# Performance work log

Measured on AMD Instinct MI355X. Metric: run time of the kernel, lower is better.

## Reference

```python
import jax, jax.numpy as jnp
import numpy as np

D_MODEL = 1024
N_HEADS = 16
D_HEAD = D_MODEL // N_HEADS
WIN = 128        # local_window
HALF = WIN // 2  # 64
KW = 2 * WIN     # kv window length per block (half-left + block + half-right)


def setup_inputs() -> dict:
    key = jax.random.key(0)
    ks = jax.random.split(key, 6)
    B, L = 2, 8192
    s = 0.02
    return {
        "x": jax.random.normal(ks[0], (B, L, D_MODEL), dtype=jnp.float32),
        "wq": jax.random.normal(ks[1], (D_MODEL, D_MODEL), dtype=jnp.float32) * s,
        "wk": jax.random.normal(ks[2], (D_MODEL, D_MODEL), dtype=jnp.float32) * s,
        "wv": jax.random.normal(ks[3], (D_MODEL, D_MODEL), dtype=jnp.float32) * s,
        "wo": jax.random.normal(ks[4], (D_MODEL, D_MODEL), dtype=jnp.float32) * s,
        "bo": jax.random.normal(ks[5], (D_MODEL,), dtype=jnp.float32) * s,
    }


def _rotate_half(t):
    t1, t2 = jnp.split(t, 2, axis=-1)
    return jnp.concatenate([-t2, t1], axis=-1)


def _rope(L, dtype):
    inv_freq = 1.0 / (10000.0 ** (jnp.arange(0, D_HEAD, 2, dtype=jnp.float32) / D_HEAD))
    t = jnp.arange(L, dtype=jnp.float32)
    freqs = t[:, None] * inv_freq[None, :]          # [L, D_HEAD/2]
    emb = jnp.concatenate([freqs, freqs], axis=-1)  # [L, D_HEAD]
    return jnp.cos(emb).astype(dtype), jnp.sin(emb).astype(dtype)


def reference(x, wq, wk, wv, wo, bo):
    B, L, D = x.shape
    H, Dh = N_HEADS, D_HEAD
    # projections (torch Linear: x @ W.T)
    q = (x @ wq.T).reshape(B, L, H, Dh).transpose(0, 2, 1, 3)  # [B,H,L,Dh]
    k = (x @ wk.T).reshape(B, L, H, Dh).transpose(0, 2, 1, 3)
    v = (x @ wv.T).reshape(B, L, H, Dh).transpose(0, 2, 1, 3)
    cos, sin = _rope(L, x.dtype)                    # [L, Dh]
    q = q * cos + _rotate_half(q) * sin
    k = k * cos + _rotate_half(k) * sin
    nb = L // WIN
    starts = jnp.arange(nb) * WIN - HALF            # window start per block
    idx = starts[:, None] + jnp.arange(KW)          # [nb, KW] kv indices
    valid = (idx >= 0) & (idx < L)
    idxc = jnp.clip(idx, 0, L - 1)
    kw = k[:, :, idxc]                              # [B,H,nb,KW,Dh]
    vw = v[:, :, idxc]
    qb = q.reshape(B, H, nb, WIN, Dh)
    scores = jnp.einsum('bhnqd,bhnkd->bhnqk', qb, kw) / np.sqrt(Dh).astype(x.dtype)
    scores = jnp.where(valid[None, None, :, None, :], scores, -jnp.inf)
    attn = jax.nn.softmax(scores, axis=-1)
    out = jnp.einsum('bhnqk,bhnkd->bhnqd', attn, vw).reshape(B, H, L, Dh)
    out = out.transpose(0, 2, 1, 3).reshape(B, L, D)
    return out @ wo.T + bo
```

## Files before the change

### kernel.cpp

```cpp
#include <hip/hip_runtime.h>
#include <cstdint>
#include <math.h>

#define L_SEQ 8192
#define DM    1024
#define NQK   2048

typedef unsigned short u16;
typedef __bf16 bf16;
typedef bf16  bf16x8 __attribute__((ext_vector_type(8)));
typedef float f32x4  __attribute__((ext_vector_type(4)));

__device__ __forceinline__ u16 f2bf(float f) {
    unsigned u = __float_as_uint(f);
    u += 0x7fffu + ((u >> 16) & 1u);
    return (u16)(u >> 16);
}

__device__ __forceinline__ f32x4 mfma16(bf16x8 a, bf16x8 b, f32x4 c) {
    return __builtin_amdgcn_mfma_f32_16x16x32_bf16(a, b, c, 0, 0, 0);
}

__device__ __forceinline__ void gld_lds16(const u16* g, u16* l) {
    __builtin_amdgcn_global_load_lds((const __attribute__((address_space(1))) void*)g,
                                     (__attribute__((address_space(3))) void*)l,
                                     16, 0, 0);
}

__global__ void cvt_bf16(const float* __restrict__ src, u16* __restrict__ dst, int n8) {
    int i = blockIdx.x * 256 + threadIdx.x;
    if (i >= n8) return;
    const float4* s4 = (const float4*)src;
    float4 a = s4[2 * i], b = s4[2 * i + 1];
    union { uint4 u; u16 h[8]; } r;
    r.h[0] = f2bf(a.x); r.h[1] = f2bf(a.y); r.h[2] = f2bf(a.z); r.h[3] = f2bf(a.w);
    r.h[4] = f2bf(b.x); r.h[5] = f2bf(b.y); r.h[6] = f2bf(b.z); r.h[7] = f2bf(b.w);
    ((uint4*)dst)[i] = r.u;
}

__global__ void rope_tbl(float2* __restrict__ t) {
    int idx = blockIdx.x * 256 + threadIdx.x;
    int pos = idx >> 5, i = idx & 31;
    float invf = exp2f(-0.4152410118609191f * (float)i);
    float s, c;
    sincosf((float)pos * invf, &s, &c);
    t[idx] = make_float2(c, s);
}


#define QITER(U, WIMM, RD, ST) do {                                            \
    __builtin_amdgcn_s_waitcnt(WIMM);                                          \
    __builtin_amdgcn_sched_barrier(0);                                         \
    __builtin_amdgcn_s_barrier();                                              \
    __builtin_amdgcn_sched_barrier(0);                                         \
    if (RD) {                                                                  \
        _Pragma("unroll")                                                      \
        for (int m = 0; m < 8; m++)                                            \
            fA[(U + 1) & 1][m] = *(const bf16x8*)(SAs + ((U + 1) % 3) * 8192 + aBase + m * 512); \
        _Pragma("unroll")                                                      \
        for (int n = 0; n < 4; n++)                                            \
            fB[(U + 1) & 1][n] = *(const bf16x8*)(SBs + ((U + 1) % 3) * 4096 + bBase + n * 512); \
    }                                                                          \
    if (ST) {                                                                  \
        _Pragma("unroll")                                                      \
        for (int i = 0; i < 4; ++i)                                            \
            gld_lds16(gA[i] + (U + 3) * 32, ldsAt + (U % 3) * 8192 + i * 2048);\
        _Pragma("unroll")                                                      \
        for (int i = 0; i < 2; ++i)                                            \
            gld_lds16(gB[i] + (U + 3) * 32, ldsBt + (U % 3) * 4096 + i * 2048);\
    }                                                                          \
    __builtin_amdgcn_sched_barrier(0);                                         \
    __builtin_amdgcn_s_setprio(1);                                             \
    _Pragma("unroll")                                                          \
    for (int m = 0; m < 8; m++)                                                \
        _Pragma("unroll")                                                      \
        for (int n = 0; n < 4; n++)                                            \
            acc[m][n] = mfma16(fA[(U) & 1][m], fB[(U) & 1][n], acc[m][n]);     \
    __builtin_amdgcn_s_setprio(0);                                             \
    __builtin_amdgcn_sched_barrier(0);                                         \
} while (0)

#define K_LOOP_ALL()                                                           \
    QITER(0,0x0076,1,1);  QITER(1,0x0076,1,1);  QITER(2,0x0076,1,1);           \
    QITER(3,0x0076,1,1);  QITER(4,0x0076,1,1);  QITER(5,0x0076,1,1);           \
    QITER(6,0x0076,1,1);  QITER(7,0x0076,1,1);  QITER(8,0x0076,1,1);           \
    QITER(9,0x0076,1,1);  QITER(10,0x0076,1,1); QITER(11,0x0076,1,1);          \
    QITER(12,0x0076,1,1); QITER(13,0x0076,1,1); QITER(14,0x0076,1,1);          \
    QITER(15,0x0076,1,1); QITER(16,0x0076,1,1); QITER(17,0x0076,1,1);          \
    QITER(18,0x0076,1,1); QITER(19,0x0076,1,1); QITER(20,0x0076,1,1);          \
    QITER(21,0x0076,1,1); QITER(22,0x0076,1,1); QITER(23,0x0076,1,1);          \
    QITER(24,0x0076,1,1); QITER(25,0x0076,1,1); QITER(26,0x0076,1,1);          \
    QITER(27,0x0076,1,1); QITER(28,0x0076,1,1); QITER(29,0x0076,1,0);          \
    QITER(30,0x0070,1,0); QITER(31,0x0070,0,0)

#define GEMM_SETUP()                                                           \
    u16* SAs = smem;                                \
    u16* SBs = smem + 24576;                        \
    const int tid = threadIdx.x;                                               \
    const int lane = tid & 63, w = tid >> 6;                                   \
    const int wm = w >> 1, wn = w & 1;                                         \
    const int quad = lane >> 4, ln = lane & 15;                                \
    const u16* gA[4]; const u16* gB[2];                                        \
    _Pragma("unroll")                                                          \
    for (int i = 0; i < 4; ++i) {                                              \
        int s = i * 256 + tid;                                                 \
        int li = s >> 3, pc = s & 7, lc = pc ^ (li & 7);                       \
        int row = 2 * li + (lc >> 2), kc = lc & 3;                             \
        gA[i] = Ap + (size_t)(m0 + row) * DM + kc * 8;                         \
    }                                                                          \
    _Pragma("unroll")                                                          \
    for (int i = 0; i < 2; ++i) {                                              \
        int s = i * 256 + tid;                                                 \
        int li = s >> 3, pc = s & 7, lc = pc ^ (li & 7);                       \
        int row = 2 * li + (lc >> 2), kc = lc & 3;                             \
        gB[i] = Bp + (size_t)(n0 + row) * DM + kc * 8;                         \
    }                                                                          \
    u16* ldsAt = SAs + tid * 8;                                                \
    u16* ldsBt = SBs + tid * 8;                                                \
    const int l7  = (ln >> 1) & 7;                                             \
    const int pcq = ((ln & 1) * 4 + quad) ^ l7;                                \
    const int aBase = (wm * 64 + (ln >> 1)) * 64 + pcq * 8;                    \
    const int bBase = (wn * 32 + (ln >> 1)) * 64 + pcq * 8;                    \
    const f32x4 fz = {0.f, 0.f, 0.f, 0.f};                                     \
    f32x4 acc[8][4];                                                           \
    _Pragma("unroll")                                                          \
    for (int a = 0; a < 8; a++)                                                \
        _Pragma("unroll")                                                      \
        for (int b = 0; b < 4; b++) acc[a][b] = fz;                            \
    bf16x8 fA[2][8], fB[2][4];                                                 \
                              \
    _Pragma("unroll")                                                          \
    for (int t3 = 0; t3 < 3; ++t3) {                                           \
        _Pragma("unroll")                                                      \
        for (int i = 0; i < 4; ++i) gld_lds16(gA[i] + t3 * 32, ldsAt + t3 * 8192 + i * 2048); \
        _Pragma("unroll")                                                      \
        for (int i = 0; i < 2; ++i) gld_lds16(gB[i] + t3 * 32, ldsBt + t3 * 4096 + i * 2048); \
    }                                                                          \
    __builtin_amdgcn_s_waitcnt(0x0F7C);        \
    __builtin_amdgcn_s_barrier();                                              \
    __builtin_amdgcn_sched_barrier(0);                                         \
    _Pragma("unroll")                                                          \
    for (int m = 0; m < 8; m++) fA[0][m] = *(const bf16x8*)(SAs + aBase + m * 512); \
    _Pragma("unroll")                                                          \
    for (int n = 0; n < 4; n++) fB[0][n] = *(const bf16x8*)(SBs + bBase + n * 512)

__global__ __launch_bounds__(256, 2) void gemm_qkv_fused(
    const u16* __restrict__ X,
    const u16* __restrict__ W,
    const float2* __restrict__ rope,
    u16* __restrict__ Y,
    u16* __restrict__ Vt)
{
    __shared__ __align__(16) u16 smem[36864];

    const int o   = (int)blockIdx.x;
    const int xcd = o & 7;
    const int r   = o >> 3;
    const int st  = r >> 6;
    const int t   = r & 63;
    const int m0  = (xcd * 8 + (t & 7)) * 256;
    const int n0  = (st * 8 + (t >> 3)) * 128;

    const u16* Ap = X;
    const u16* Bp = W;
    GEMM_SETUP();
    K_LOOP_ALL();
    __syncthreads();

    if (n0 < 2048) {
        #pragma unroll
        for (int mt = 0; mt < 8; mt++)
            #pragma unroll
            for (int reg = 0; reg < 4; reg++) {
                int rg = (m0 + wm * 128 + mt * 16 + quad * 4 + reg) & (L_SEQ - 1);
                const float2* rp = rope + rg * 32;
                #pragma unroll
                for (int nt = 0; nt < 2; nt++) {
                    float2 cs = rp[nt * 16 + ln];
                    float x1 = acc[mt][nt][reg], x2 = acc[mt][nt + 2][reg];
                    acc[mt][nt][reg]     = x1 * cs.x - x2 * cs.y;
                    acc[mt][nt + 2][reg] = x2 * cs.x + x1 * cs.y;
                }
            }
        u16* Es = smem;
        #pragma unroll
        for (int mh = 0; mh < 2; mh++) {
            if (mh) __syncthreads();
            if (wm == mh) {
                #pragma unroll
                for (int mt = 0; mt < 8; mt++)
                    #pragma unroll
                    for (int nt = 0; nt < 4; nt++)
                        #pragma unroll
                        for (int reg = 0; reg < 4; reg++)
                            Es[(mt * 16 + quad * 4 + reg) * 136 + wn * 64 + nt * 16 + ln] =
                                f2bf(acc[mt][nt][reg]);
            }
            __syncthreads();
            #pragma unroll
            for (int i = 0; i < 8; i++) {
                int idx = i * 256 + tid;
                int row = idx >> 4, ch = (idx & 15) * 8;
                uint4 v = *(const uint4*)(Es + row * 136 + ch);
                *(uint4*)(Y + (size_t)(m0 + mh * 128 + row) * NQK + n0 + ch) = v;
            }
        }
    } else {
        u16* Es = smem;
        const int bb = m0 >> 13, seq0 = m0 & (L_SEQ - 1);
        #pragma unroll
        for (int rh = 0; rh < 2; rh++) {
            if (rh) __syncthreads();
            if (wm == rh) {
                #pragma unroll
                for (int mt = 0; mt < 8; mt++)
                    #pragma unroll
                    for (int nt = 0; nt < 4; nt++)
                        #pragma unroll
                        for (int reg = 0; reg < 4; reg++)
                            Es[(wn * 64 + nt * 16 + ln) * 136 + mt * 16 + quad * 4 + reg] =
                                f2bf(acc[mt][nt][reg]);
            }
            __syncthreads();
            #pragma unroll
            for (int i = 0; i < 8; i++) {
                int idx = i * 256 + tid;
                int dr = idx >> 4, ch = (idx & 15) * 8;
                int gc = n0 - 2048 + dr;
                uint4 v = *(const uint4*)(Es + dr * 136 + ch);
                *(uint4*)(Vt + (size_t)(bb * 1024 + gc) * L_SEQ + seq0 + rh * 128 + ch) = v;
            }
        }
    }
}

__global__ __launch_bounds__(256, 2) void gemm_oproj(
    const u16* __restrict__ A,
    const u16* __restrict__ Wo,
    const float* __restrict__ bias,
    float* __restrict__ Out)
{
    __shared__ __align__(16) u16 smem[36864];

    const int o   = (int)blockIdx.x;
    const int xcd = o & 7;
    const int t   = o >> 3;
    const int m0  = (xcd * 8 + (t & 7)) * 256;
    const int n0  = (t >> 3) * 128;

    const u16* Ap = A;
    const u16* Bp = Wo;
    GEMM_SETUP();
    K_LOOP_ALL();
    __syncthreads();

    float b4[4];
    #pragma unroll
    for (int nt = 0; nt < 4; nt++) b4[nt] = bias[n0 + wn * 64 + nt * 16 + ln];

    float* Ef = (float*)smem;
    #pragma unroll
    for (int mq = 0; mq < 4; mq++) {
        if (mq) __syncthreads();
        if (wm == (mq >> 1)) {
            #pragma unroll
            for (int mt = 0; mt < 4; mt++)
                #pragma unroll
                for (int nt = 0; nt < 4; nt++)
                    #pragma unroll
                    for (int reg = 0; reg < 4; reg++)
                        Ef[(mt * 16 + quad * 4 + reg) * 132 + wn * 64 + nt * 16 + ln] =
                            acc[(mq & 1) * 4 + mt][nt][reg] + b4[nt];
        }
        __syncthreads();
        #pragma unroll
        for (int i = 0; i < 8; i++) {
            int idx = i * 256 + tid;
            int row = idx >> 5, ch = (idx & 31) * 4;
            float4 v = *(const float4*)(Ef + row * 132 + ch);
            *(float4*)(Out + (size_t)(m0 + mq * 64 + row) * DM + n0 + ch) = v;
        }
    }
}

__global__ __launch_bounds__(512, 4) void attn(
    const u16* __restrict__ QK,
    const u16* __restrict__ Vt,
    u16* __restrict__ AO)
{
    __shared__ __align__(16) u16 Ks[256 * 64];
    __shared__ __align__(16) u16 Vs[64 * 256];
    __shared__ __align__(16) u16 pbuf[8][512];

    const int blk = blockIdx.x;
    const int h   = blockIdx.y;
    const int b   = blockIdx.z;
    const int tid = threadIdx.x;
    const int lane = tid & 63, w = tid >> 6;
    const int quad = lane >> 4, ln = lane & 15;
    const int wstart = blk * 128 - 64;
    const size_t bbase = (size_t)b * L_SEQ;

    const u16* Kg = QK + 1024 + h * 64;
    const u16* Vg = Vt + (size_t)(b * 1024 + h * 64) * L_SEQ;

    #pragma unroll
    for (int i = 0; i < 4; i++) {
        int c = i * 512 + tid;
        int row = c >> 3, cl = c & 7, cg = cl ^ (row & 7);
        int kr = wstart + row;
        kr = kr < 0 ? 0 : (kr > L_SEQ - 1 ? L_SEQ - 1 : kr);
        gld_lds16(Kg + (size_t)(bbase + kr) * NQK + cg * 8, Ks + c * 8);
    }
    #pragma unroll
    for (int i = 0; i < 4; i++) {
        int c = i * 512 + tid;
        int d = c >> 5, kc = c & 31, cg = kc ^ (d & 7);
        int key = wstart + cg * 8;
        key = key < 0 ? 0 : (key > L_SEQ - 8 ? L_SEQ - 8 : key);
        gld_lds16(Vg + (size_t)d * L_SEQ + key, Vs + c * 8);
    }

    const int qrow = blk * 128 + w * 16 + ln;
    const u16* qp = QK + (bbase + qrow) * NQK + h * 64 + quad * 8;
    bf16x8 aq0 = *(const bf16x8*)qp;
    bf16x8 aq1 = *(const bf16x8*)(qp + 32);
    __syncthreads();

    const f32x4 fz = {0.f, 0.f, 0.f, 0.f};
    f32x4 s[16];
    #pragma unroll
    for (int nt = 0; nt < 16; nt++) {
        int row = nt * 16 + ln;
        bf16x8 b0 = *(const bf16x8*)(Ks + row * 64 + ((quad       ^ (ln & 7)) * 8));
        bf16x8 b1 = *(const bf16x8*)(Ks + row * 64 + (((4 + quad) ^ (ln & 7)) * 8));
        f32x4 t = mfma16(aq0, b0, fz);
        t = mfma16(aq1, b1, t);
        s[nt] = t;
    }
    __syncthreads();

    const float SC = 0.125f * 1.4426950408889634f;
    float mr[4] = {-INFINITY, -INFINITY, -INFINITY, -INFINITY};
    #pragma unroll
    for (int nt = 0; nt < 16; nt++) {
        int key = wstart + nt * 16 + ln;
        bool valid = (key >= 0) && (key < L_SEQ);
        #pragma unroll
        for (int r = 0; r < 4; r++) {
            float v = valid ? s[nt][r] * SC : -INFINITY;
            s[nt][r] = v;
            mr[r] = fmaxf(mr[r], v);
        }
    }
    #pragma unroll
    for (int off = 1; off < 16; off <<= 1)
        #pragma unroll
        for (int r = 0; r < 4; r++) mr[r] = fmaxf(mr[r], __shfl_xor(mr[r], off));

    float lr[4] = {0.f, 0.f, 0.f, 0.f};
    #pragma unroll
    for (int nt = 0; nt < 16; nt++)
        #pragma unroll
        for (int r = 0; r < 4; r++) {
            float p = exp2f(s[nt][r] - mr[r]);
            s[nt][r] = p;
            lr[r] += p;
        }
    #pragma unroll
    for (int off = 1; off < 16; off <<= 1)
        #pragma unroll
        for (int r = 0; r < 4; r++) lr[r] += __shfl_xor(lr[r], off);
    float rl[4];
    #pragma unroll
    for (int r = 0; r < 4; r++) rl[r] = 1.f / lr[r];

    u16* pb = pbuf[w];
    f32x4 o[4] = {fz, fz, fz, fz};
    #pragma unroll
    for (int ks = 0; ks < 8; ks++) {
        #pragma unroll
        for (int n2 = 0; n2 < 2; n2++) {
            int nt = ks * 2 + n2;
            #pragma unroll
            for (int r = 0; r < 4; r++)
                pb[(quad * 4 + r) * 32 + ((n2 * 16 + ln) ^ (quad * 8))] = f2bf(s[nt][r]);
        }
        bf16x8 ap = *(const bf16x8*)(pb + ln * 32 + ((quad * 8) ^ (((ln >> 2) & 3) * 8)));
        #pragma unroll
        for (int dt = 0; dt < 4; dt++) {
            int d = dt * 16 + ln;
            bf16x8 vb = *(const bf16x8*)(Vs + d * 256 + (((ks * 4 + quad) ^ (ln & 7)) * 8));
            o[dt] = mfma16(ap, vb, o[dt]);
        }
    }

    u16* AOs = Ks;
    #pragma unroll
    for (int dt = 0; dt < 4; dt++)
        #pragma unroll
        for (int r = 0; r < 4; r++)
            AOs[(w * 16 + quad * 4 + r) * 72 + dt * 16 + ln] = f2bf(o[dt][r] * rl[r]);
    __syncthreads();
    #pragma unroll
    for (int i = 0; i < 2; i++) {
        int c = i * 512 + tid;
        int row = c >> 3, ch = (c & 7) * 8;
        uint4 v = *(const uint4*)(AOs + row * 72 + ch);
        *(uint4*)(AO + (bbase + blk * 128 + row) * DM + h * 64 + ch) = v;
    }
}

extern "C" void kernel_launch(void* const* d_in, const int* in_sizes, int n_in,
                              void* d_out, int out_size, void* d_ws, size_t ws_size,
                              hipStream_t stream) {
    const float* x  = (const float*)d_in[0];
    const float* wq = (const float*)d_in[1];
    const float* wk = (const float*)d_in[2];
    const float* wv = (const float*)d_in[3];
    const float* wo = (const float*)d_in[4];
    const float* bo = (const float*)d_in[5];
    float* out = (float*)d_out;

    char* ws = (char*)d_ws;
    const size_t MB = 1024 * 1024;
    u16*   xb  = (u16*)ws;
    u16*   fqk = (u16*)(ws + 32 * MB);
    u16*   vt  = (u16*)(ws + 96 * MB);
    u16*   wf  = (u16*)(ws + 128 * MB);
    float2* rt = (float2*)(ws + 134 * MB);
    u16*   wob = (u16*)(ws + 136 * MB);
    u16*   aob = xb;

    cvt_bf16<<<8192, 256, 0, stream>>>(x, xb, 2097152);
    cvt_bf16<<<512, 256, 0, stream>>>(wq, wf, 131072);
    cvt_bf16<<<512, 256, 0, stream>>>(wk, wf + 1024 * 1024, 131072);
    cvt_bf16<<<512, 256, 0, stream>>>(wv, wf + 2 * 1024 * 1024, 131072);
    cvt_bf16<<<512, 256, 0, stream>>>(wo, wob, 131072);
    rope_tbl<<<1024, 256, 0, stream>>>(rt);

    gemm_qkv_fused<<<1536, 256, 0, stream>>>(xb, wf, rt, fqk, vt);
    attn<<<dim3(64, 16, 2), 512, 0, stream>>>(fqk, vt, aob);
    gemm_oproj<<<512, 256, 0, stream>>>(aob, wob, bo, out);
}
```

Measured before the change: 365.7 us.

## Merge prep kernels, split QKV GEMM into QK and V kernels, refine attention sync

Folds the four weight-conversion launches and the rope table launch into a single prep kernel to cut launch count. Splits the fused QKV GEMM into separate QK (with RoPE) and V (transposed store) kernels, which removes the per-block branch at the cost of one extra launch. In attention, the Q fragment loads are issued before the K/V async copies, __syncthreads is replaced with explicit waitcnt plus barrier so the V load can overlap the QK^T and softmax, and MFMA sections get raised wave priority. The V-only kernel keeps the blockIdx-to-tile mapping, which may change tile scheduling balance.

```diff
diff --git a/kernel.cpp b/kernel.cpp
--- a/kernel.cpp
+++ b/kernel.cpp
@@ -38,15 +38,82 @@
     ((uint4*)dst)[i] = r.u;
 }
 
-__global__ void rope_tbl(float2* __restrict__ t) {
+__global__ void prep_misc(const float* __restrict__ wq, const float* __restrict__ wk,
+                          const float* __restrict__ wv, const float* __restrict__ wo,
+                          u16* __restrict__ wf, u16* __restrict__ wob,
+                          float2* __restrict__ rt) {
     int idx = blockIdx.x * 256 + threadIdx.x;
-    int pos = idx >> 5, i = idx & 31;
-    float invf = exp2f(-0.4152410118609191f * (float)i);
-    float s, c;
-    sincosf((float)pos * invf, &s, &c);
-    t[idx] = make_float2(c, s);
-}
-
+    if (idx < 524288) {
+        int sel = idx >> 17, i = idx & 131071;
+        const float* s = sel == 0 ? wq : sel == 1 ? wk : sel == 2 ? wv : wo;
+        u16* d        = sel == 0 ? wf : sel == 1 ? wf + 1048576 : sel == 2 ? wf + 2097152 : wob;
+        const float4* s4 = (const float4*)s;
+        float4 a = s4[2 * i], b = s4[2 * i + 1];
+        union { uint4 u; u16 h[8]; } r;
+        r.h[0] = f2bf(a.x); r.h[1] = f2bf(a.y); r.h[2] = f2bf(a.z); r.h[3] = f2bf(a.w);
+        r.h[4] = f2bf(b.x); r.h[5] = f2bf(b.y); r.h[6] = f2bf(b.z); r.h[7] = f2bf(b.w);
+        ((uint4*)d)[i] = r.u;
+    } else {
+        int j = idx - 524288;
+        int pos = j >> 5, i = j & 31;
+        float invf = exp2f(-0.4152410118609191f * (float)i);
+        float s, c;
+        sincosf((float)pos * invf, &s, &c);
+        rt[j] = make_float2(c, s);
+    }
+}
+
+
+#define STAGE_COMMON()                                                         \
+    const int tid = threadIdx.x;                                               \
+    const int lane = tid & 63, w = tid >> 6;                                   \
+    const int wm = w >> 1, wn = w & 1;                                         \
+    const u16* gA[4]; const u16* gB[2];                                        \
+    _Pragma("unroll")                                                          \
+    for (int i = 0; i < 4; ++i) {                                              \
+        int s = i * 256 + tid;                                                 \
+        int li = s >> 3, pc = s & 7, lc = pc ^ (li & 7);                       \
+        int row = 2 * li + (lc >> 2), kc = lc & 3;                             \
+        gA[i] = Ap + (size_t)(m0 + row) * DM + kc * 8;                         \
+    }                                                                          \
+    _Pragma("unroll")                                                          \
+    for (int i = 0; i < 2; ++i) {                                              \
+        int s = i * 256 + tid;                                                 \
+        int li = s >> 3, pc = s & 7, lc = pc ^ (li & 7);                       \
+        int row = 2 * li + (lc >> 2), kc = lc & 3;                             \
+        gB[i] = Bp + (size_t)(n0 + row) * DM + kc * 8;                         \
+    }                                                                          \
+    u16* ldsAt = SAs + tid * 8;                                                \
+    u16* ldsBt = SBs + tid * 8;                                                \
+                              \
+    _Pragma("unroll")                                                          \
+    for (int t3 = 0; t3 < 3; ++t3) {                                           \
+        _Pragma("unroll")                                                      \
+        for (int i = 0; i < 4; ++i) gld_lds16(gA[i] + t3 * 32, ldsAt + t3 * 8192 + i * 2048); \
+        _Pragma("unroll")                                                      \
+        for (int i = 0; i < 2; ++i) gld_lds16(gB[i] + t3 * 32, ldsBt + t3 * 4096 + i * 2048); \
+    }
+
+#define GEMM16_PRE()                                                           \
+    const int quad = lane >> 4, ln = lane & 15;                                \
+    const int l7  = (ln >> 1) & 7;                                             \
+    const int pcq = ((ln & 1) * 4 + quad) ^ l7;                                \
+    const int aBase = (wm * 64 + (ln >> 1)) * 64 + pcq * 8;                    \
+    const int bBase = (wn * 32 + (ln >> 1)) * 64 + pcq * 8;                    \
+    const f32x4 fz = {0.f, 0.f, 0.f, 0.f};                                     \
+    f32x4 acc[8][4];                                                           \
+    _Pragma("unroll")                                                          \
+    for (int a = 0; a < 8; a++)                                                \
+        _Pragma("unroll")                                                      \
+        for (int b = 0; b < 4; b++) acc[a][b] = fz;                            \
+    bf16x8 fA[2][8], fB[2][4];                                                 \
+    __builtin_amdgcn_s_waitcnt(0x0F7C);        \
+    __builtin_amdgcn_s_barrier();                                              \
+    __builtin_amdgcn_sched_barrier(0);                                         \
+    _Pragma("unroll")                                                          \
+    for (int m = 0; m < 8; m++) fA[0][m] = *(const bf16x8*)(SAs + aBase + m * 512); \
+    _Pragma("unroll")                                                          \
+    for (int n = 0; n < 4; n++) fB[0][n] = *(const bf16x8*)(SBs + bBase + n * 512)
 
 #define QITER(U, WIMM, RD, ST) do {                                            \
     __builtin_amdgcn_s_waitcnt(WIMM);                                          \
@@ -93,65 +160,15 @@
     QITER(27,0x0076,1,1); QITER(28,0x0076,1,1); QITER(29,0x0076,1,0);          \
     QITER(30,0x0070,1,0); QITER(31,0x0070,0,0)
 
-#define GEMM_SETUP()                                                           \
-    u16* SAs = smem;                                \
-    u16* SBs = smem + 24576;                        \
-    const int tid = threadIdx.x;                                               \
-    const int lane = tid & 63, w = tid >> 6;                                   \
-    const int wm = w >> 1, wn = w & 1;                                         \
-    const int quad = lane >> 4, ln = lane & 15;                                \
-    const u16* gA[4]; const u16* gB[2];                                        \
-    _Pragma("unroll")                                                          \
-    for (int i = 0; i < 4; ++i) {                                              \
-        int s = i * 256 + tid;                                                 \
-        int li = s >> 3, pc = s & 7, lc = pc ^ (li & 7);                       \
-        int row = 2 * li + (lc >> 2), kc = lc & 3;                             \
-        gA[i] = Ap + (size_t)(m0 + row) * DM + kc * 8;                         \
-    }                                                                          \
-    _Pragma("unroll")                                                          \
-    for (int i = 0; i < 2; ++i) {                                              \
-        int s = i * 256 + tid;                                                 \
-        int li = s >> 3, pc = s & 7, lc = pc ^ (li & 7);                       \
-        int row = 2 * li + (lc >> 2), kc = lc & 3;                             \
-        gB[i] = Bp + (size_t)(n0 + row) * DM + kc * 8;                         \
-    }                                                                          \
-    u16* ldsAt = SAs + tid * 8;                                                \
-    u16* ldsBt = SBs + tid * 8;                                                \
-    const int l7  = (ln >> 1) & 7;                                             \
-    const int pcq = ((ln & 1) * 4 + quad) ^ l7;                                \
-    const int aBase = (wm * 64 + (ln >> 1)) * 64 + pcq * 8;                    \
-    const int bBase = (wn * 32 + (ln >> 1)) * 64 + pcq * 8;                    \
-    const f32x4 fz = {0.f, 0.f, 0.f, 0.f};                                     \
-    f32x4 acc[8][4];                                                           \
-    _Pragma("unroll")                                                          \
-    for (int a = 0; a < 8; a++)                                                \
-        _Pragma("unroll")                                                      \
-        for (int b = 0; b < 4; b++) acc[a][b] = fz;                            \
-    bf16x8 fA[2][8], fB[2][4];                                                 \
-                              \
-    _Pragma("unroll")                                                          \
-    for (int t3 = 0; t3 < 3; ++t3) {                                           \
-        _Pragma("unroll")                                                      \
-        for (int i = 0; i < 4; ++i) gld_lds16(gA[i] + t3 * 32, ldsAt + t3 * 8192 + i * 2048); \
-        _Pragma("unroll")                                                      \
-        for (int i = 0; i < 2; ++i) gld_lds16(gB[i] + t3 * 32, ldsBt + t3 * 4096 + i * 2048); \
-    }                                                                          \
-    __builtin_amdgcn_s_waitcnt(0x0F7C);        \
-    __builtin_amdgcn_s_barrier();                                              \
-    __builtin_amdgcn_sched_barrier(0);                                         \
-    _Pragma("unroll")                                                          \
-    for (int m = 0; m < 8; m++) fA[0][m] = *(const bf16x8*)(SAs + aBase + m * 512); \
-    _Pragma("unroll")                                                          \
-    for (int n = 0; n < 4; n++) fB[0][n] = *(const bf16x8*)(SBs + bBase + n * 512)
-
-__global__ __launch_bounds__(256, 2) void gemm_qkv_fused(
+__global__ __launch_bounds__(256, 2) void gemm_qk(
     const u16* __restrict__ X,
     const u16* __restrict__ W,
     const float2* __restrict__ rope,
-    u16* __restrict__ Y,
-    u16* __restrict__ Vt)
+    u16* __restrict__ Y)
 {
     __shared__ __align__(16) u16 smem[36864];
+    u16* SAs = smem;
+    u16* SBs = smem + 24576;
 
     const int o   = (int)blockIdx.x;
     const int xcd = o & 7;
@@ -163,73 +180,95 @@
 
     const u16* Ap = X;
     const u16* Bp = W;
-    GEMM_SETUP();
+    STAGE_COMMON();
+    GEMM16_PRE();
     K_LOOP_ALL();
     __syncthreads();
 
-    if (n0 < 2048) {
-        #pragma unroll
-        for (int mt = 0; mt < 8; mt++)
+    #pragma unroll
+    for (int mt = 0; mt < 8; mt++)
+        #pragma unroll
+        for (int reg = 0; reg < 4; reg++) {
+            int rg = (m0 + wm * 128 + mt * 16 + quad * 4 + reg) & (L_SEQ - 1);
+            const float2* rp = rope + rg * 32;
             #pragma unroll
-            for (int reg = 0; reg < 4; reg++) {
-                int rg = (m0 + wm * 128 + mt * 16 + quad * 4 + reg) & (L_SEQ - 1);
-                const float2* rp = rope + rg * 32;
+            for (int nt = 0; nt < 2; nt++) {
+                float2 cs = rp[nt * 16 + ln];
+                float x1 = acc[mt][nt][reg], x2 = acc[mt][nt + 2][reg];
+                acc[mt][nt][reg]     = x1 * cs.x - x2 * cs.y;
+                acc[mt][nt + 2][reg] = x2 * cs.x + x1 * cs.y;
+            }
+        }
+    u16* Es = smem;
+    #pragma unroll
+    for (int mh = 0; mh < 2; mh++) {
+        if (mh) __syncthreads();
+        if (wm == mh) {
+            #pragma unroll
+            for (int mt = 0; mt < 8; mt++)
                 #pragma unroll
-                for (int nt = 0; nt < 2; nt++) {
-                    float2 cs = rp[nt * 16 + ln];
-                    float x1 = acc[mt][nt][reg], x2 = acc[mt][nt + 2][reg];
-                    acc[mt][nt][reg]     = x1 * cs.x - x2 * cs.y;
-                    acc[mt][nt + 2][reg] = x2 * cs.x + x1 * cs.y;
-                }
-            }
-        u16* Es = smem;
-        #pragma unroll
-        for (int mh = 0; mh < 2; mh++) {
-            if (mh) __syncthreads();
-            if (wm == mh) {
+                for (int nt = 0; nt < 4; nt++)
+                    #pragma unroll
+                    for (int reg = 0; reg < 4; reg++)
+                        Es[(mt * 16 + quad * 4 + reg) * 136 + wn * 64 + nt * 16 + ln] =
+                            f2bf(acc[mt][nt][reg]);
+        }
+        __syncthreads();
+        #pragma unroll
+        for (int i = 0; i < 8; i++) {
+            int idx = i * 256 + tid;
+            int row = idx >> 4, ch = (idx & 15) * 8;
+            uint4 v = *(const uint4*)(Es + row * 136 + ch);
+            *(uint4*)(Y + (size_t)(m0 + mh * 128 + row) * NQK + n0 + ch) = v;
+        }
+    }
+}
+
+__global__ __launch_bounds__(256, 2) void gemm_v(
+    const u16* __restrict__ X,
+    const u16* __restrict__ W,
+    u16* __restrict__ Vt)
+{
+    __shared__ __align__(16) u16 smem[36864];
+    u16* SAs = smem;
+    u16* SBs = smem + 24576;
+
+    const int o   = (int)blockIdx.x;
+    const int xcd = o & 7;
+    const int t   = o >> 3;
+    const int m0  = (xcd * 8 + (t & 7)) * 256;
+    const int n0  = 2048 + (t >> 3) * 128;
+
+    const u16* Ap = X;
+    const u16* Bp = W;
+    STAGE_COMMON();
+    GEMM16_PRE();
+    K_LOOP_ALL();
+    __syncthreads();
+
+    u16* Es = smem;
+    const int bb = m0 >> 13, seq0 = m0 & (L_SEQ - 1);
+    #pragma unroll
+    for (int rh = 0; rh < 2; rh++) {
+        if (rh) __syncthreads();
+        if (wm == rh) {
+            #pragma unroll
+            for (int mt = 0; mt < 8; mt++)
                 #pragma unroll
-                for (int mt = 0; mt < 8; mt++)
+                for (int nt = 0; nt < 4; nt++)
                     #pragma unroll
-                    for (int nt = 0; nt < 4; nt++)
-                        #pragma unroll
-                        for (int reg = 0; reg < 4; reg++)
-                            Es[(mt * 16 + quad * 4 + reg) * 136 + wn * 64 + nt * 16 + ln] =
-                                f2bf(acc[mt][nt][reg]);
-            }
-            __syncthreads();
-            #pragma unroll
-            for (int i = 0; i < 8; i++) {
-                int idx = i * 256 + tid;
-                int row = idx >> 4, ch = (idx & 15) * 8;
-                uint4 v = *(const uint4*)(Es + row * 136 + ch);
-                *(uint4*)(Y + (size_t)(m0 + mh * 128 + row) * NQK + n0 + ch) = v;
-            }
-        }
-    } else {
-        u16* Es = smem;
-        const int bb = m0 >> 13, seq0 = m0 & (L_SEQ - 1);
-        #pragma unroll
-        for (int rh = 0; rh < 2; rh++) {
-            if (rh) __syncthreads();
-            if (wm == rh) {
-                #pragma unroll
-                for (int mt = 0; mt < 8; mt++)
-                    #pragma unroll
-                    for (int nt = 0; nt < 4; nt++)
-                        #pragma unroll
-                        for (int reg = 0; reg < 4; reg++)
-                            Es[(wn * 64 + nt * 16 + ln) * 136 + mt * 16 + quad * 4 + reg] =
-                                f2bf(acc[mt][nt][reg]);
-            }
-            __syncthreads();
-            #pragma unroll
-            for (int i = 0; i < 8; i++) {
-                int idx = i * 256 + tid;
-                int dr = idx >> 4, ch = (idx & 15) * 8;
-                int gc = n0 - 2048 + dr;
-                uint4 v = *(const uint4*)(Es + dr * 136 + ch);
-                *(uint4*)(Vt + (size_t)(bb * 1024 + gc) * L_SEQ + seq0 + rh * 128 + ch) = v;
-            }
+                    for (int reg = 0; reg < 4; reg++)
+                        Es[(wn * 64 + nt * 16 + ln) * 136 + mt * 16 + quad * 4 + reg] =
+                            f2bf(acc[mt][nt][reg]);
+        }
+        __syncthreads();
+        #pragma unroll
+        for (int i = 0; i < 8; i++) {
+            int idx = i * 256 + tid;
+            int dr = idx >> 4, ch = (idx & 15) * 8;
+            int gc = n0 - 2048 + dr;
+            uint4 v = *(const uint4*)(Es + dr * 136 + ch);
+            *(uint4*)(Vt + (size_t)(bb * 1024 + gc) * L_SEQ + seq0 + rh * 128 + ch) = v;
         }
     }
 }
@@ -241,6 +280,8 @@
     float* __restrict__ Out)
 {
     __shared__ __align__(16) u16 smem[36864];
+    u16* SAs = smem;
+    u16* SBs = smem + 24576;
 
     const int o   = (int)blockIdx.x;
     const int xcd = o & 7;
@@ -250,7 +291,8 @@
 
     const u16* Ap = A;
     const u16* Bp = Wo;
-    GEMM_SETUP();
+    STAGE_COMMON();
+    GEMM16_PRE();
     K_LOOP_ALL();
     __syncthreads();
 
@@ -304,6 +346,11 @@
     const u16* Kg = QK + 1024 + h * 64;
     const u16* Vg = Vt + (size_t)(b * 1024 + h * 64) * L_SEQ;
 
+    const int qrow = blk * 128 + w * 16 + ln;
+    const u16* qp = QK + (bbase + qrow) * NQK + h * 64 + quad * 8;
+    bf16x8 aq0 = *(const bf16x8*)qp;
+    bf16x8 aq1 = *(const bf16x8*)(qp + 32);
+
     #pragma unroll
     for (int i = 0; i < 4; i++) {
         int c = i * 512 + tid;
@@ -321,14 +368,13 @@
         gld_lds16(Vg + (size_t)d * L_SEQ + key, Vs + c * 8);
     }
 
-    const int qrow = blk * 128 + w * 16 + ln;
-    const u16* qp = QK + (bbase + qrow) * NQK + h * 64 + quad * 8;
-    bf16x8 aq0 = *(const bf16x8*)qp;
-    bf16x8 aq1 = *(const bf16x8*)(qp + 32);
-    __syncthreads();
+    __builtin_amdgcn_s_waitcnt(0x0F74);
+    __builtin_amdgcn_s_barrier();
+    __builtin_amdgcn_sched_barrier(0);
 
     const f32x4 fz = {0.f, 0.f, 0.f, 0.f};
     f32x4 s[16];
+    __builtin_amdgcn_s_setprio(1);
     #pragma unroll
     for (int nt = 0; nt < 16; nt++) {
         int row = nt * 16 + ln;
@@ -338,7 +384,7 @@
         t = mfma16(aq1, b1, t);
         s[nt] = t;
     }
-    __syncthreads();
+    __builtin_amdgcn_s_setprio(0);
 
     const float SC = 0.125f * 1.4426950408889634f;
     float mr[4] = {-INFINITY, -INFINITY, -INFINITY, -INFINITY};
@@ -375,8 +421,13 @@
     #pragma unroll
     for (int r = 0; r < 4; r++) rl[r] = 1.f / lr[r];
 
+    __builtin_amdgcn_s_waitcnt(0x0F70);
+    __builtin_amdgcn_s_barrier();
+    __builtin_amdgcn_sched_barrier(0);
+
     u16* pb = pbuf[w];
     f32x4 o[4] = {fz, fz, fz, fz};
+    __builtin_amdgcn_s_setprio(1);
     #pragma unroll
     for (int ks = 0; ks < 8; ks++) {
         #pragma unroll
@@ -394,6 +445,7 @@
             o[dt] = mfma16(ap, vb, o[dt]);
         }
     }
+    __builtin_amdgcn_s_setprio(0);
 
     u16* AOs = Ks;
     #pragma unroll
@@ -433,13 +485,10 @@
     u16*   aob = xb;
 
     cvt_bf16<<<8192, 256, 0, stream>>>(x, xb, 2097152);
-    cvt_bf16<<<512, 256, 0, stream>>>(wq, wf, 131072);
-    cvt_bf16<<<512, 256, 0, stream>>>(wk, wf + 1024 * 1024, 131072);
-    cvt_bf16<<<512, 256, 0, stream>>>(wv, wf + 2 * 1024 * 1024, 131072);
-    cvt_bf16<<<512, 256, 0, stream>>>(wo, wob, 131072);
-    rope_tbl<<<1024, 256, 0, stream>>>(rt);
-
-    gemm_qkv_fused<<<1536, 256, 0, stream>>>(xb, wf, rt, fqk, vt);
+    prep_misc<<<3072, 256, 0, stream>>>(wq, wk, wv, wo, wf, wob, rt);
+
+    gemm_qk<<<1024, 256, 0, stream>>>(xb, wf, rt, fqk);
+    gemm_v<<<512, 256, 0, stream>>>(xb, wf, vt);
     attn<<<dim3(64, 16, 2), 512, 0, stream>>>(fqk, vt, aob);
     gemm_oproj<<<512, 256, 0, stream>>>(aob, wob, bo, out);
 }
```

New measurement: 358.6 us. About the same (-1.9%).
